# Kernel tuning notes

Measured on AMD Instinct MI355X. Metric: run time of the kernel, lower is better.

The kernel has to match this reference:

```python
import jax, jax.numpy as jnp
import numpy as np

N = 4096            # nodes
LMAX = 6
NUM_COEF = (LMAX + 1) ** 2   # 49 SH coefficients
RES = 18            # S2 grid resolution (lat = lon = 18)
C = 128             # num_channels


def setup_inputs() -> dict:
    key = jax.random.key(0)
    k1, k2, k3, k4 = jax.random.split(key, 4)
    return {
        "inputs": jax.random.normal(k1, (N, NUM_COEF, 2 * C), dtype=jnp.float32),
        "scalars": jax.random.normal(k2, (N, 3 * C), dtype=jnp.float32),
        # SO3Grid projection matrices (precomputed SH-basis grids in the real module)
        "to_grid_mat": jax.random.normal(k3, (RES, RES, NUM_COEF), dtype=jnp.float32) / np.sqrt(NUM_COEF).astype(np.float32),
        "from_grid_mat": jax.random.normal(k4, (RES, RES, NUM_COEF), dtype=jnp.float32) / np.float32(RES),
    }


def reference(inputs, scalars, to_grid_mat, from_grid_mat):
    # inputs:  [N, (lmax+1)^2, 2C]; scalars: [N, 3C]
    n, k, c2 = inputs.shape
    s = scalars[:, None, :]                       # [N, 1, 3C]
    # Type-0 path part 1: SwiGLU on first 2C scalars -> [N, 1, C]
    a, b = jnp.split(s[..., :c2], 2, axis=-1)
    output_scalars = jax.nn.silu(a) * b
    # Type-0 path part 2: sigmoid gate on last C scalars -> [N, 1, C]
    gate_scalars = jax.nn.sigmoid(s[..., c2:])
    # Type-L path: project to S2 grid -> [N, RES, RES, 2C]
    x_grid = jnp.einsum('pqi,nic->npqc', to_grid_mat, inputs)
    # chunk-multiply gating (self tensor product) -> [N, RES, RES, C]
    x1, x2 = jnp.split(x_grid, 2, axis=-1)
    x_grid = x1 * x2
    # project back to SH coefficients -> [N, (lmax+1)^2, C]
    output_vectors = jnp.einsum('pqi,npqc->nic', from_grid_mat, x_grid)
    output_vectors = output_vectors * gate_scalars
    # merge: add SwiGLU scalars onto the l=0 component
    return output_vectors.at[:, 0:1, :].add(output_scalars)
```

## Files before the change

### kernel.cpp

```cpp
#include <hip/hip_runtime.h>


#define KC    49
#define PQ    324
#define NPX   12544
#define OUTK  6272
#define NTILE 11
#define TROWS 325
#define TCOLS 68
#define FROWS 50
#define FCOLS 356
#define TTOT  (TROWS * TCOLS)
#define FTOT  (FROWS * FCOLS)
#define WTOT  (TTOT + FTOT)
#define WPAD  39904

typedef __attribute__((ext_vector_type(8)))  short bf16x8;
typedef __attribute__((ext_vector_type(4)))  short bf16x4;
typedef __attribute__((ext_vector_type(16))) float f32x16;
typedef __attribute__((ext_vector_type(4)))  unsigned int u32x4;

__device__ __forceinline__ unsigned int cvtpk_bf16(float lo, float hi) {
    unsigned int r;
    asm("v_cvt_pk_bf16_f32 %0, %1, %2" : "=v"(r) : "v"(lo), "v"(hi));
    return r;
}
__device__ __forceinline__ unsigned short f2bf(float f) {
    unsigned u = __builtin_bit_cast(unsigned, f);
    return (unsigned short)((u + 0x7FFFu + ((u >> 16) & 1u)) >> 16);
}
__device__ __forceinline__ bf16x8 ld8(const unsigned short* p) {
    const bf16x4 lo = *(const bf16x4*)p;
    const bf16x4 hi = *(const bf16x4*)(p + 4);
    bf16x8 r;
    r[0] = lo[0]; r[1] = lo[1]; r[2] = lo[2]; r[3] = lo[3];
    r[4] = hi[0]; r[5] = hi[1]; r[6] = hi[2]; r[7] = hi[3];
    return r;
}

__global__ void prep_kernel(const float* __restrict__ Tg, const float* __restrict__ Fg,
                            unsigned short* __restrict__ W)
{
    const int idx = blockIdx.x * 256 + threadIdx.x;
    if (idx < TTOT) {
        const int r = idx / TCOLS, i = idx % TCOLS;
        const float v = (r < PQ && i < KC) ? Tg[r * KC + i] : 0.0f;
        W[idx] = f2bf(v);
    } else if (idx < WPAD) {
        float v = 0.0f;
        if (idx < WTOT) {
            const int idx2 = idx - TTOT;
            const int k = idx2 / FCOLS, p = idx2 % FCOLS;
            if (k < KC && p < PQ) v = Fg[p * KC + k];
        }
        W[idx] = f2bf(v);
    }
}

__global__ __launch_bounds__(512, 4)
void s2_fused(const float* __restrict__ X,
              const float* __restrict__ S,
              const unsigned short* __restrict__ W,
              float* __restrict__ out,
              int nit)
{
    __shared__ __align__(16) unsigned short lds[WPAD];

    const int tid = threadIdx.x;
    for (int idx = tid; idx < WPAD / 8; idx += 512) {
        const u32x4 v = *(const u32x4*)(W + (size_t)idx * 8);
        *(u32x4*)(lds + (size_t)idx * 8) = v;
    }
    __syncthreads();

    const int w  = tid >> 6;
    const int l  = tid & 63;
    const int cl = l & 31;
    const int hb = l >> 5;
    const int cs = w >> 1;
    const int nw = w & 1;

    const unsigned short* tw  = lds;
    const unsigned short* fw0 = lds + TTOT + (size_t)cl * FCOLS;
    const unsigned short* fw1 = lds + TTOT + (size_t)min(cl + 32, KC) * FCOLS;

    const int nbase = blockIdx.x * (2 * nit) + nw;

    for (int it = 0; it < nit; ++it) {
        const int n = nbase + 2 * it;

        const float* xp = X + (size_t)n * NPX + 32 * cs + cl;
        const float* sp = S + (size_t)n * 384 + 32 * cs + cl;
        const float sraw0 = sp[0], sraw1 = sp[128], sraw2 = sp[256];
        const float sg  = 1.0f / (1.0f + __expf(-sraw2));
        const float osc = (sraw0 / (1.0f + __expf(-sraw0))) * sraw1;

        bf16x8 bx[2][4];
        {
            float ch[4][16];
#pragma unroll
            for (int xi = 0; xi < 2; ++xi)
#pragma unroll
            for (int j = 0; j < 8; ++j) {
                const int i = 8 * hb + j;
                ch[0][8 * xi + j] = (i < KC) ? xp[128 * xi + (size_t)i * 256] : 0.0f;
            }
#pragma unroll
            for (int st = 0; st < 4; ++st) {
                if (st < 3) {
#pragma unroll
                    for (int xi = 0; xi < 2; ++xi)
#pragma unroll
                    for (int j = 0; j < 8; ++j) {
                        const int i = 16 * (st + 1) + 8 * hb + j;
                        ch[st + 1][8 * xi + j] = (i < KC) ? xp[128 * xi + (size_t)i * 256] : 0.0f;
                    }
                }
#pragma unroll
                for (int xi = 0; xi < 2; ++xi) {
                    u32x4 d;
#pragma unroll
                    for (int p = 0; p < 4; ++p)
                        d[p] = cvtpk_bf16(ch[st][8 * xi + 2 * p], ch[st][8 * xi + 2 * p + 1]);
                    bx[xi][st] = __builtin_bit_cast(bf16x8, d);
                }
            }
        }

        f32x16 accO0, accO1;
#pragma unroll
        for (int r = 0; r < 16; ++r) { accO0[r] = 0.0f; accO1[r] = 0.0f; }

#pragma unroll 2
        for (int t = 0; t < NTILE; ++t) {
            const int trow = min(32 * t + cl, 324);
            const unsigned short* twt = tw + trow * TCOLS + 8 * hb;
            const bf16x8 ta0 = ld8(twt);
            const bf16x8 ta1 = ld8(twt + 16);
            const bf16x8 ta2 = ld8(twt + 32);
            const bf16x8 ta3 = ld8(twt + 48);

            f32x16 ac0, ac1;
#pragma unroll
            for (int r = 0; r < 16; ++r) { ac0[r] = 0.0f; ac1[r] = 0.0f; }
            ac0 = __builtin_amdgcn_mfma_f32_32x32x16_bf16(ta0, bx[0][0], ac0, 0, 0, 0);
            ac1 = __builtin_amdgcn_mfma_f32_32x32x16_bf16(ta0, bx[1][0], ac1, 0, 0, 0);
            ac0 = __builtin_amdgcn_mfma_f32_32x32x16_bf16(ta1, bx[0][1], ac0, 0, 0, 0);
            ac1 = __builtin_amdgcn_mfma_f32_32x32x16_bf16(ta1, bx[1][1], ac1, 0, 0, 0);
            ac0 = __builtin_amdgcn_mfma_f32_32x32x16_bf16(ta2, bx[0][2], ac0, 0, 0, 0);
            ac1 = __builtin_amdgcn_mfma_f32_32x32x16_bf16(ta2, bx[1][2], ac1, 0, 0, 0);
            ac0 = __builtin_amdgcn_mfma_f32_32x32x16_bf16(ta3, bx[0][3], ac0, 0, 0, 0);
            ac1 = __builtin_amdgcn_mfma_f32_32x32x16_bf16(ta3, bx[1][3], ac1, 0, 0, 0);

            unsigned int q0 = cvtpk_bf16(ac0[0]  * ac1[0],  ac0[1]  * ac1[1]);
            unsigned int q1 = cvtpk_bf16(ac0[2]  * ac1[2],  ac0[3]  * ac1[3]);
            unsigned int q2 = cvtpk_bf16(ac0[4]  * ac1[4],  ac0[5]  * ac1[5]);
            unsigned int q3 = cvtpk_bf16(ac0[6]  * ac1[6],  ac0[7]  * ac1[7]);
            unsigned int q4 = cvtpk_bf16(ac0[8]  * ac1[8],  ac0[9]  * ac1[9]);
            unsigned int q5 = cvtpk_bf16(ac0[10] * ac1[10], ac0[11] * ac1[11]);
            unsigned int q6 = cvtpk_bf16(ac0[12] * ac1[12], ac0[13] * ac1[13]);
            unsigned int q7 = cvtpk_bf16(ac0[14] * ac1[14], ac0[15] * ac1[15]);

            asm("v_permlane32_swap_b32 %0, %1" : "+v"(q0), "+v"(q2));
            asm("v_permlane32_swap_b32 %0, %1" : "+v"(q1), "+v"(q3));
            asm("v_permlane32_swap_b32 %0, %1" : "+v"(q4), "+v"(q6));
            asm("v_permlane32_swap_b32 %0, %1" : "+v"(q5), "+v"(q7));
            u32x4 b0v, b1v;
            b0v[0] = q0; b0v[1] = q1; b0v[2] = q2; b0v[3] = q3;
            b1v[0] = q4; b1v[1] = q5; b1v[2] = q6; b1v[3] = q7;
            const bf16x8 bg0 = __builtin_bit_cast(bf16x8, b0v);
            const bf16x8 bg1 = __builtin_bit_cast(bf16x8, b1v);

            const int fcol = 32 * t + 8 * hb;
            const bf16x8 fa00 = ld8(fw0 + fcol);
            const bf16x8 fa01 = ld8(fw0 + fcol + 16);
            const bf16x8 fa10 = ld8(fw1 + fcol);
            const bf16x8 fa11 = ld8(fw1 + fcol + 16);

            accO0 = __builtin_amdgcn_mfma_f32_32x32x16_bf16(fa00, bg0, accO0, 0, 0, 0);
            accO1 = __builtin_amdgcn_mfma_f32_32x32x16_bf16(fa10, bg0, accO1, 0, 0, 0);
            accO0 = __builtin_amdgcn_mfma_f32_32x32x16_bf16(fa01, bg1, accO0, 0, 0, 0);
            accO1 = __builtin_amdgcn_mfma_f32_32x32x16_bf16(fa11, bg1, accO1, 0, 0, 0);
        }

        float* op = out + (size_t)n * OUTK + 32 * cs + cl;
#pragma unroll
        for (int r = 0; r < 16; ++r) {
            const int k0 = (r & 3) + 8 * (r >> 2) + 4 * hb;
            float v = sg * accO0[r];
            if (k0 == 0) v += osc;
            op[(size_t)k0 * 128] = v;
            const int k1 = 32 + k0;
            if (k1 < KC) op[(size_t)k1 * 128] = sg * accO1[r];
        }
    }
}

extern "C" void kernel_launch(void* const* d_in, const int* in_sizes, int n_in,
                              void* d_out, int out_size, void* d_ws, size_t ws_size,
                              hipStream_t stream) {
    const float* inputs  = (const float*)d_in[0];
    const float* scalars = (const float*)d_in[1];
    const float* Tg      = (const float*)d_in[2];
    const float* Fg      = (const float*)d_in[3];
    float* outp          = (float*)d_out;

    unsigned short* W = (unsigned short*)d_ws;

    const int N = in_sizes[1] / 384;
    hipLaunchKernelGGL(prep_kernel, dim3((WPAD + 255) / 256), dim3(256), 0, stream,
                       Tg, Fg, W);

    const int nit  = 4;
    const int grid = N / (2 * nit);
    hipLaunchKernelGGL(s2_fused, dim3(grid), dim3(512), 0, stream,
                       inputs, scalars, W, outp, nit);
}
```

Before: 115.5 us.

## Stage input rows through LDS as bf16 with coalesced float4 loads

Each iteration now loads two nodes' input tiles cooperatively with float4 loads, converts them to bf16, and stores them into a new LDS staging buffer. Waves then gather their MFMA B-operands from LDS instead of issuing strided scalar global loads. The change also passes a zero accumulator as a runtime argument, splits the weight loads into smaller groups, and hoists the from-grid weight loads ahead of the gating math. The LDS footprint grows to about 144KB, which lowers occupancy (launch bounds drop to 2), and it adds two block barriers per iteration.

```diff
diff --git a/kernel.cpp b/kernel.cpp
--- a/kernel.cpp
+++ b/kernel.cpp
@@ -14,11 +14,14 @@
 #define FTOT  (FROWS * FCOLS)
 #define WTOT  (TTOT + FTOT)
 #define WPAD  39904
+#define XBN   16384
+#define LDSE  (WPAD + 2 * XBN)
 
 typedef __attribute__((ext_vector_type(8)))  short bf16x8;
 typedef __attribute__((ext_vector_type(4)))  short bf16x4;
 typedef __attribute__((ext_vector_type(16))) float f32x16;
 typedef __attribute__((ext_vector_type(4)))  unsigned int u32x4;
+typedef __attribute__((ext_vector_type(2)))  unsigned int u32x2;
 
 __device__ __forceinline__ unsigned int cvtpk_bf16(float lo, float hi) {
     unsigned int r;
@@ -57,21 +60,21 @@
     }
 }
 
-__global__ __launch_bounds__(512, 4)
+__global__ __launch_bounds__(512, 2)
 void s2_fused(const float* __restrict__ X,
               const float* __restrict__ S,
               const unsigned short* __restrict__ W,
               float* __restrict__ out,
-              int nit)
+              int nit,
+              float fzero)
 {
-    __shared__ __align__(16) unsigned short lds[WPAD];
+    __shared__ __align__(16) unsigned short lds[LDSE];
 
     const int tid = threadIdx.x;
     for (int idx = tid; idx < WPAD / 8; idx += 512) {
         const u32x4 v = *(const u32x4*)(W + (size_t)idx * 8);
         *(u32x4*)(lds + (size_t)idx * 8) = v;
     }
-    __syncthreads();
 
     const int w  = tid >> 6;
     const int l  = tid & 63;
@@ -83,13 +86,31 @@
     const unsigned short* tw  = lds;
     const unsigned short* fw0 = lds + TTOT + (size_t)cl * FCOLS;
     const unsigned short* fw1 = lds + TTOT + (size_t)min(cl + 32, KC) * FCOLS;
-
-    const int nbase = blockIdx.x * (2 * nit) + nw;
+    unsigned short* XB = lds + WPAD;
+
+    f32x16 Z;
+#pragma unroll
+    for (int r = 0; r < 16; ++r) Z[r] = fzero;
 
     for (int it = 0; it < nit; ++it) {
-        const int n = nbase + 2 * it;
-
-        const float* xp = X + (size_t)n * NPX + 32 * cs + cl;
+        const int base = blockIdx.x * (2 * nit) + 2 * it;
+
+        for (int q = tid; q < 8192; q += 512) {
+            const int nq  = q >> 12;
+            const int rem = q & 4095;
+            const int i   = rem >> 6;
+            const int c4  = (rem & 63) << 2;
+            float4 v = make_float4(0.f, 0.f, 0.f, 0.f);
+            if (i < KC)
+                v = *(const float4*)(X + (size_t)(base + nq) * NPX + i * 256 + c4);
+            u32x2 d;
+            d[0] = cvtpk_bf16(v.x, v.y);
+            d[1] = cvtpk_bf16(v.z, v.w);
+            *(u32x2*)(XB + nq * XBN + i * 256 + c4) = d;
+        }
+        __syncthreads();
+
+        const int n = base + nw;
         const float* sp = S + (size_t)n * 384 + 32 * cs + cl;
         const float sraw0 = sp[0], sraw1 = sp[128], sraw2 = sp[256];
         const float sg  = 1.0f / (1.0f + __expf(-sraw2));
@@ -97,60 +118,51 @@
 
         bf16x8 bx[2][4];
         {
-            float ch[4][16];
+            const unsigned short* xb = XB + nw * XBN + 32 * cs + cl;
 #pragma unroll
             for (int xi = 0; xi < 2; ++xi)
 #pragma unroll
-            for (int j = 0; j < 8; ++j) {
-                const int i = 8 * hb + j;
-                ch[0][8 * xi + j] = (i < KC) ? xp[128 * xi + (size_t)i * 256] : 0.0f;
+            for (int st = 0; st < 4; ++st) {
+                bf16x8 t;
+#pragma unroll
+                for (int j = 0; j < 8; ++j)
+                    t[j] = (short)xb[(16 * st + 8 * hb + j) * 256 + 128 * xi];
+                bx[xi][st] = t;
             }
-#pragma unroll
-            for (int st = 0; st < 4; ++st) {
-                if (st < 3) {
-#pragma unroll
-                    for (int xi = 0; xi < 2; ++xi)
-#pragma unroll
-                    for (int j = 0; j < 8; ++j) {
-                        const int i = 16 * (st + 1) + 8 * hb + j;
-                        ch[st + 1][8 * xi + j] = (i < KC) ? xp[128 * xi + (size_t)i * 256] : 0.0f;
-                    }
-                }
-#pragma unroll
-                for (int xi = 0; xi < 2; ++xi) {
-                    u32x4 d;
-#pragma unroll
-                    for (int p = 0; p < 4; ++p)
-                        d[p] = cvtpk_bf16(ch[st][8 * xi + 2 * p], ch[st][8 * xi + 2 * p + 1]);
-                    bx[xi][st] = __builtin_bit_cast(bf16x8, d);
-                }
-            }
-        }
+        }
+        __syncthreads();
 
         f32x16 accO0, accO1;
 #pragma unroll
         for (int r = 0; r < 16; ++r) { accO0[r] = 0.0f; accO1[r] = 0.0f; }
 
-#pragma unroll 2
         for (int t = 0; t < NTILE; ++t) {
             const int trow = min(32 * t + cl, 324);
             const unsigned short* twt = tw + trow * TCOLS + 8 * hb;
-            const bf16x8 ta0 = ld8(twt);
-            const bf16x8 ta1 = ld8(twt + 16);
-            const bf16x8 ta2 = ld8(twt + 32);
-            const bf16x8 ta3 = ld8(twt + 48);
 
             f32x16 ac0, ac1;
-#pragma unroll
-            for (int r = 0; r < 16; ++r) { ac0[r] = 0.0f; ac1[r] = 0.0f; }
-            ac0 = __builtin_amdgcn_mfma_f32_32x32x16_bf16(ta0, bx[0][0], ac0, 0, 0, 0);
-            ac1 = __builtin_amdgcn_mfma_f32_32x32x16_bf16(ta0, bx[1][0], ac1, 0, 0, 0);
-            ac0 = __builtin_amdgcn_mfma_f32_32x32x16_bf16(ta1, bx[0][1], ac0, 0, 0, 0);
-            ac1 = __builtin_amdgcn_mfma_f32_32x32x16_bf16(ta1, bx[1][1], ac1, 0, 0, 0);
-            ac0 = __builtin_amdgcn_mfma_f32_32x32x16_bf16(ta2, bx[0][2], ac0, 0, 0, 0);
-            ac1 = __builtin_amdgcn_mfma_f32_32x32x16_bf16(ta2, bx[1][2], ac1, 0, 0, 0);
-            ac0 = __builtin_amdgcn_mfma_f32_32x32x16_bf16(ta3, bx[0][3], ac0, 0, 0, 0);
-            ac1 = __builtin_amdgcn_mfma_f32_32x32x16_bf16(ta3, bx[1][3], ac1, 0, 0, 0);
+            {
+                const bf16x8 ta0 = ld8(twt);
+                const bf16x8 ta1 = ld8(twt + 16);
+                ac0 = __builtin_amdgcn_mfma_f32_32x32x16_bf16(ta0, bx[0][0], Z, 0, 0, 0);
+                ac1 = __builtin_amdgcn_mfma_f32_32x32x16_bf16(ta0, bx[1][0], Z, 0, 0, 0);
+                ac0 = __builtin_amdgcn_mfma_f32_32x32x16_bf16(ta1, bx[0][1], ac0, 0, 0, 0);
+                ac1 = __builtin_amdgcn_mfma_f32_32x32x16_bf16(ta1, bx[1][1], ac1, 0, 0, 0);
+            }
+            {
+                const bf16x8 ta2 = ld8(twt + 32);
+                const bf16x8 ta3 = ld8(twt + 48);
+                ac0 = __builtin_amdgcn_mfma_f32_32x32x16_bf16(ta2, bx[0][2], ac0, 0, 0, 0);
+                ac1 = __builtin_amdgcn_mfma_f32_32x32x16_bf16(ta2, bx[1][2], ac1, 0, 0, 0);
+                ac0 = __builtin_amdgcn_mfma_f32_32x32x16_bf16(ta3, bx[0][3], ac0, 0, 0, 0);
+                ac1 = __builtin_amdgcn_mfma_f32_32x32x16_bf16(ta3, bx[1][3], ac1, 0, 0, 0);
+            }
+
+            const int fcol = 32 * t + 8 * hb;
+            const bf16x8 fa00 = ld8(fw0 + fcol);
+            const bf16x8 fa01 = ld8(fw0 + fcol + 16);
+            const bf16x8 fa10 = ld8(fw1 + fcol);
+            const bf16x8 fa11 = ld8(fw1 + fcol + 16);
 
             unsigned int q0 = cvtpk_bf16(ac0[0]  * ac1[0],  ac0[1]  * ac1[1]);
             unsigned int q1 = cvtpk_bf16(ac0[2]  * ac1[2],  ac0[3]  * ac1[3]);
@@ -171,12 +183,6 @@
             const bf16x8 bg0 = __builtin_bit_cast(bf16x8, b0v);
             const bf16x8 bg1 = __builtin_bit_cast(bf16x8, b1v);
 
-            const int fcol = 32 * t + 8 * hb;
-            const bf16x8 fa00 = ld8(fw0 + fcol);
-            const bf16x8 fa01 = ld8(fw0 + fcol + 16);
-            const bf16x8 fa10 = ld8(fw1 + fcol);
-            const bf16x8 fa11 = ld8(fw1 + fcol + 16);
-
             accO0 = __builtin_amdgcn_mfma_f32_32x32x16_bf16(fa00, bg0, accO0, 0, 0, 0);
             accO1 = __builtin_amdgcn_mfma_f32_32x32x16_bf16(fa10, bg0, accO1, 0, 0, 0);
             accO0 = __builtin_amdgcn_mfma_f32_32x32x16_bf16(fa01, bg1, accO0, 0, 0, 0);
@@ -214,5 +220,5 @@
     const int nit  = 4;
     const int grid = N / (2 * nit);
     hipLaunchKernelGGL(s2_fused, dim3(grid), dim3(512), 0, stream,
-                       inputs, scalars, W, outp, nit);
-}
+                       inputs, scalars, W, outp, nit, 0.0f);
+}
```

Measured after the change: 143.5 us. +24.2%, slower.
